# Kernel optimization log

Hardware: AMD Instinct MI355X
Metric: run time of the kernel (lower is better)

The kernel has to match this reference:

```python
import jax, jax.numpy as jnp
import numpy as np

N, F_NODE, F_EDGE = 1024, 64, 32
F_IN = 2 * F_NODE + F_EDGE  # 160


def setup_inputs() -> dict:
    key = jax.random.key(0)
    ks = jax.random.split(key, 6)
    H = jax.random.normal(ks[0], (N, F_NODE), dtype=jnp.float32)
    A = jax.random.randint(ks[1], (N, N), 0, 2).astype(jnp.float32)
    E = jax.random.normal(ks[2], (N, N, F_EDGE), dtype=jnp.float32)
    # params: reset_parameters_uniform -> U(-s, s), s = 1/sqrt(dim0)
    s = 1.0 / np.sqrt(F_IN)
    W = jax.random.uniform(ks[3], (F_IN, F_NODE), jnp.float32, -s, s)
    W_att = jax.random.uniform(ks[4], (F_IN, F_NODE), jnp.float32, -s, s)
    sb = 1.0 / np.sqrt(F_NODE)
    bias = jax.random.uniform(ks[5], (F_NODE,), jnp.float32, -sb, sb)
    return {"H": H, "A": A, "E": E, "W": W, "W_att": W_att, "bias": bias}


def reference(H, A, E, W, W_att, bias):
    n = H.shape[0]
    # all-pairs concat: HE[a,b] = [H[a], H[b], E[a,b]]  -> [N, N, 2F+Fe]
    H_row = jnp.broadcast_to(H[:, None, :], (n, n, H.shape[1]))  # H2: repeat over dim 1
    H_col = jnp.broadcast_to(H[None, :, :], (n, n, H.shape[1]))  # H1: repeat over dim 0
    HE = jnp.concatenate([H_row, H_col, E], axis=2) * A[:, :, None]
    Hp = jnp.einsum('abi,ij->abj', HE, W) + bias
    Ha = jnp.einsum('abi,ij->abj', HE, W_att) + bias
    gated = jax.nn.relu(Hp) * jax.nn.sigmoid(Ha)
    return jnp.sum(gated, axis=1)
```

## Files before the change

kernel.cpp:

```cpp
#include <hip/hip_runtime.h>

#define NN 1024
#define FN 64
#define FE 32
#define FIN 160

#pragma clang diagnostic ignored "-Waddress-space-conversion"

typedef __bf16 bf16x8 __attribute__((ext_vector_type(8)));
typedef short  short8 __attribute__((ext_vector_type(8)));
typedef float  f32x4  __attribute__((ext_vector_type(4)));
typedef __attribute__((address_space(1))) const unsigned int gu32;
typedef __attribute__((address_space(3))) unsigned int lu32;

static __device__ __forceinline__ unsigned short f2b(float x){
    unsigned int u = __float_as_uint(x);
    unsigned int r = (u + 0x7fffu + ((u >> 16) & 1u)) >> 16;
    return (unsigned short)r;
}

static __device__ __forceinline__ float fast_sigmoid(float y){
    return __builtin_amdgcn_rcpf(1.0f + __expf(-y));
}

static __device__ __forceinline__ bf16x8 ldfrag(const unsigned short* p){
    return __builtin_bit_cast(bf16x8, *(const short8*)(p));
}

static __device__ __forceinline__ unsigned packtrunc(float lo, float hi){
    return __builtin_amdgcn_perm(__float_as_uint(hi), __float_as_uint(lo), 0x07060302u);
}

#define MF(A,B,C) __builtin_amdgcn_mfma_f32_16x16x32_bf16((A),(B),(C),0,0,0)

__global__ void prep(const float* __restrict__ H, const float* __restrict__ W,
                     const float* __restrict__ Wa,
                     unsigned short* __restrict__ Hb,
                     unsigned short* __restrict__ WtE,
                     unsigned short* __restrict__ WtA){
    int bid = blockIdx.x, tid = threadIdx.x;
    if (bid < 64){
        int i = (bid*256 + tid)*4;
        float4 v = *(const float4*)(H + i);
        ushort4 o;
        o.x = f2b(v.x); o.y = f2b(v.y); o.z = f2b(v.z); o.w = f2b(v.w);
        *(ushort4*)(Hb + i) = o;
    } else {
        const float* src = (bid == 64) ? W : Wa;
        unsigned short* dst = (bid == 64) ? WtE : WtA;
        for (int idx = tid; idx < FIN*FN; idx += 256){
            int k = idx >> 6, j = idx & 63;
            dst[j*FIN + k] = f2b(src[idx]);
        }
    }
}

#define STAGE(buf_, su_) do {                                               \
    const float* gt_ = E + (size_t)a*(NN*FE) + (su_)*2048;                  \
    _Pragma("unroll")                                                       \
    for (int is_ = 0; is_ < 2; is_++){                                      \
        int L_   = is_*256 + tid;                                           \
        int row_ = ((L_>>8)&1)*32 + ((L_>>7)&1)*16 + (L_ & 15);             \
        int src_ = row_*32 + ((((L_>>4)&3)*2 + ((L_>>6)&1))*4);             \
        __builtin_amdgcn_global_load_lds(                                   \
            (gu32*)(gt_ + src_),                                            \
            (lu32*)(&Et[buf_][is_*1024 + wave*256]), 16, 0, 0);             \
    }                                                                       \
} while(0)

#define COMPMT(buf_, su_, mt_) do {                                         \
    const float* tp_ = &Et[buf_][(mh*2 + (mt_))*512 + quad*64 + col*4];     \
    float4 v0_ = *(const float4*)(tp_);                                     \
    float4 v1_ = *(const float4*)(tp_ + 256);                               \
    int gr_ = (su_)*64 + mh*32 + (mt_)*16 + col;                            \
    bf16x8 hh0_ = ldfrag(Hb + gr_*FN + quad*8);                             \
    bf16x8 hh1_ = ldfrag(Hb + gr_*FN + 32 + quad*8);                        \
    int4 pk_;                                                               \
    pk_.x = (int)packtrunc(v0_.x, v0_.y);                                   \
    pk_.y = (int)packtrunc(v0_.z, v0_.w);                                   \
    pk_.z = (int)packtrunc(v1_.x, v1_.y);                                   \
    pk_.w = (int)packtrunc(v1_.z, v1_.w);                                   \
    bf16x8 ef_ = __builtin_bit_cast(bf16x8, pk_);                           \
    _Pragma("unroll")                                                       \
    for (int tl = 0; tl < 2; tl++){                                         \
        f32x4 pw_ = MF(ef_, Bw[tl][2], MF(hh1_, Bw[tl][1],                  \
                     MF(hh0_, Bw[tl][0], cw[tl])));                         \
        f32x4 pa_ = MF(ef_, Ba[tl][2], MF(hh1_, Ba[tl][1],                  \
                     MF(hh0_, Ba[tl][0], ca[tl])));                         \
        _Pragma("unroll")                                                   \
        for (int r4 = 0; r4 < 4; r4++){                                     \
            float am_ = amask[(su_)*64 + mh*32 + (mt_)*16 + quad*4 + r4];   \
            float f_  = fmaxf(pw_[r4], 0.f) * fast_sigmoid(pa_[r4]);        \
            acc[tl] += am_ * f_;                                            \
        }                                                                   \
    }                                                                       \
} while(0)

__global__ __launch_bounds__(256, 4) void mga_fused(
    const float* __restrict__ A,
    const float* __restrict__ E,
    const unsigned short* __restrict__ Hb,
    const unsigned short* __restrict__ WtE, const unsigned short* __restrict__ WtA,
    const float* __restrict__ bias, float* __restrict__ out)
{
    int a    = blockIdx.x;
    int tid  = threadIdx.x;
    int wave = tid >> 6, lane = tid & 63;
    int col  = lane & 15, quad = lane >> 4;
    int half = wave >> 1, mh = wave & 1;

    __shared__ float Et[4][2048];
    __shared__ float amask[NN];
    __shared__ int wsum[4];
    float* red = (float*)Et;

    int b0 = wave*256 + lane*4;
    float4 av = *(const float4*)(A + (size_t)a*NN + b0);

    bf16x8 Bw[2][3], Ba[2][3];
    #pragma unroll
    for (int tl = 0; tl < 2; tl++){
        int n = (2*half + tl)*16 + col;
        #pragma unroll
        for (int sg = 0; sg < 3; sg++){
            Bw[tl][sg] = ldfrag(WtE + n*FIN + (sg+2)*32 + quad*8);
            Ba[tl][sg] = ldfrag(WtA + n*FIN + (sg+2)*32 + quad*8);
        }
    }

    bf16x8 ha0 = ldfrag(Hb + a*FN + quad*8);
    bf16x8 ha1 = ldfrag(Hb + a*FN + 32 + quad*8);
    f32x4 cw[2], ca[2];
    float acc[2] = {0.f, 0.f};
    #pragma unroll
    for (int tl = 0; tl < 2; tl++){
        int n = (2*half + tl)*16 + col;
        float bj = bias[n];
        f32x4 cb = {bj, bj, bj, bj};
        bf16x8 w0 = ldfrag(WtE + n*FIN + quad*8);
        bf16x8 w1 = ldfrag(WtE + n*FIN + 32 + quad*8);
        cw[tl] = MF(ha1, w1, MF(ha0, w0, cb));
        w0 = ldfrag(WtA + n*FIN + quad*8);
        w1 = ldfrag(WtA + n*FIN + 32 + quad*8);
        ca[tl] = MF(ha1, w1, MF(ha0, w0, cb));
    }

    *(float4*)(amask + b0) = av;
    int m = 0;
    m += (av.x != 0.f) ? 1 : 0;
    m += (av.y != 0.f) ? 1 : 0;
    m += (av.z != 0.f) ? 1 : 0;
    m += (av.w != 0.f) ? 1 : 0;
    #pragma unroll
    for (int d = 1; d < 64; d <<= 1) m += __shfl_xor(m, d, 64);
    if (lane == 0) wsum[wave] = m;

    STAGE(0, 0);
    STAGE(1, 1);
    __syncthreads();
    int c1 = wsum[0] + wsum[1] + wsum[2] + wsum[3];

    #pragma unroll
    for (int su = 0; su < 16; su++){
        int buf = su & 3;
        if (su + 2 < 16) STAGE((su + 2) & 3, su + 2);
        if (su < 14)      { asm volatile("s_waitcnt vmcnt(4)" ::: "memory"); }
        else if (su == 14){ asm volatile("s_waitcnt vmcnt(2)" ::: "memory"); }
        else              { asm volatile("s_waitcnt vmcnt(0)" ::: "memory"); }
        __builtin_amdgcn_s_barrier();
        COMPMT(buf, su, 0);
        COMPMT(buf, su, 1);
    }

    #pragma unroll
    for (int tl = 0; tl < 2; tl++)
        red[(wave*4 + quad)*FN + (2*half + tl)*16 + col] = acc[tl];
    __syncthreads();
    if (tid < FN){
        int rbase = (tid >= 32) ? 8 : 0;
        float sum = 0.f;
        #pragma unroll
        for (int r = 0; r < 8; r++) sum += red[(rbase + r)*FN + tid];
        float bj = bias[tid];
        float g0 = fmaxf(bj, 0.f) * fast_sigmoid(bj);
        out[(size_t)a*FN + tid] = sum + (float)(NN - c1) * g0;
    }
}

extern "C" void kernel_launch(void* const* d_in, const int* in_sizes, int n_in,
                              void* d_out, int out_size, void* d_ws, size_t ws_size,
                              hipStream_t stream) {
    const float* H    = (const float*)d_in[0];
    const float* A    = (const float*)d_in[1];
    const float* E    = (const float*)d_in[2];
    const float* W    = (const float*)d_in[3];
    const float* Wa   = (const float*)d_in[4];
    const float* bias = (const float*)d_in[5];
    float* out = (float*)d_out;

    unsigned short* Hb   = (unsigned short*)d_ws;
    unsigned short* WtE  = Hb + NN*FN;
    unsigned short* WtA  = WtE + FN*FIN;

    prep     <<<dim3(66), dim3(256), 0, stream>>>(H, W, Wa, Hb, WtE, WtA);
    mga_fused<<<dim3(NN), dim3(256), 0, stream>>>(A, E, Hb, WtE, WtA, bias, out);
}
```

Baseline: 233.0 us.

## Precompute per-node H projections and drop H MFMAs from inner loop

```diff
diff --git a/kernel.cpp b/kernel.cpp
--- a/kernel.cpp
+++ b/kernel.cpp
@@ -55,6 +55,45 @@
     }
 }
 
+__global__ void prep2(const unsigned short* __restrict__ Hb,
+                      const unsigned short* __restrict__ WtE,
+                      const unsigned short* __restrict__ WtA,
+                      const float* __restrict__ bias,
+                      float* __restrict__ U1, float* __restrict__ V1,
+                      float* __restrict__ U2t, float* __restrict__ V2t){
+    int tid = threadIdx.x, wave = tid >> 6, lane = tid & 63;
+    int col = lane & 15, quad = lane >> 4;
+    int r0  = blockIdx.x*64 + wave*16;
+    bf16x8 h0 = ldfrag(Hb + (r0 + col)*FN + quad*8);
+    bf16x8 h1 = ldfrag(Hb + (r0 + col)*FN + 32 + quad*8);
+    #pragma unroll
+    for (int jt = 0; jt < 4; jt++){
+        int n = jt*16 + col;
+        float bj = bias[n];
+        f32x4 cb = {bj, bj, bj, bj};
+        f32x4 z  = {0.f, 0.f, 0.f, 0.f};
+        bf16x8 b0 = ldfrag(WtE + n*FIN + quad*8);
+        bf16x8 b1 = ldfrag(WtE + n*FIN + 32 + quad*8);
+        f32x4 u1 = MF(h1, b1, MF(h0, b0, cb));
+        b0 = ldfrag(WtE + n*FIN + 64 + quad*8);
+        b1 = ldfrag(WtE + n*FIN + 96 + quad*8);
+        f32x4 u2 = MF(h1, b1, MF(h0, b0, z));
+        b0 = ldfrag(WtA + n*FIN + quad*8);
+        b1 = ldfrag(WtA + n*FIN + 32 + quad*8);
+        f32x4 v1 = MF(h1, b1, MF(h0, b0, cb));
+        b0 = ldfrag(WtA + n*FIN + 64 + quad*8);
+        b1 = ldfrag(WtA + n*FIN + 96 + quad*8);
+        f32x4 v2 = MF(h1, b1, MF(h0, b0, z));
+        #pragma unroll
+        for (int r = 0; r < 4; r++){
+            U1[(r0 + quad*4 + r)*FN + n] = u1[r];
+            V1[(r0 + quad*4 + r)*FN + n] = v1[r];
+        }
+        *(f32x4*)(U2t + (size_t)n*NN + r0 + quad*4) = u2;
+        *(f32x4*)(V2t + (size_t)n*NN + r0 + quad*4) = v2;
+    }
+}
+
 #define STAGE(buf_, su_) do {                                               \
     const float* gt_ = E + (size_t)a*(NN*FE) + (su_)*2048;                  \
     _Pragma("unroll")                                                       \
@@ -72,9 +111,7 @@
     const float* tp_ = &Et[buf_][(mh*2 + (mt_))*512 + quad*64 + col*4];     \
     float4 v0_ = *(const float4*)(tp_);                                     \
     float4 v1_ = *(const float4*)(tp_ + 256);                               \
-    int gr_ = (su_)*64 + mh*32 + (mt_)*16 + col;                            \
-    bf16x8 hh0_ = ldfrag(Hb + gr_*FN + quad*8);                             \
-    bf16x8 hh1_ = ldfrag(Hb + gr_*FN + 32 + quad*8);                        \
+    int g0_ = (su_)*64 + mh*32 + (mt_)*16 + quad*4;                         \
     int4 pk_;                                                               \
     pk_.x = (int)packtrunc(v0_.x, v0_.y);                                   \
     pk_.y = (int)packtrunc(v0_.z, v0_.w);                                   \
@@ -83,13 +120,20 @@
     bf16x8 ef_ = __builtin_bit_cast(bf16x8, pk_);                           \
     _Pragma("unroll")                                                       \
     for (int tl = 0; tl < 2; tl++){                                         \
-        f32x4 pw_ = MF(ef_, Bw[tl][2], MF(hh1_, Bw[tl][1],                  \
-                     MF(hh0_, Bw[tl][0], cw[tl])));                         \
-        f32x4 pa_ = MF(ef_, Ba[tl][2], MF(hh1_, Ba[tl][1],                  \
-                     MF(hh0_, Ba[tl][0], ca[tl])));                         \
+        int n_ = (2*half + tl)*16 + col;                                    \
+        f32x4 u2_ = *(const f32x4*)(U2t + (size_t)n_*NN + g0_);             \
+        f32x4 w2_ = *(const f32x4*)(V2t + (size_t)n_*NN + g0_);             \
+        f32x4 cw_, ca_;                                                     \
         _Pragma("unroll")                                                   \
         for (int r4 = 0; r4 < 4; r4++){                                     \
-            float am_ = amask[(su_)*64 + mh*32 + (mt_)*16 + quad*4 + r4];   \
+            cw_[r4] = u1s[tl] + u2_[r4];                                    \
+            ca_[r4] = v1s[tl] + w2_[r4];                                    \
+        }                                                                   \
+        f32x4 pw_ = MF(ef_, Bw[tl], cw_);                                   \
+        f32x4 pa_ = MF(ef_, Ba[tl], ca_);                                   \
+        _Pragma("unroll")                                                   \
+        for (int r4 = 0; r4 < 4; r4++){                                     \
+            float am_ = amask[g0_ + r4];                                    \
             float f_  = fmaxf(pw_[r4], 0.f) * fast_sigmoid(pa_[r4]);        \
             acc[tl] += am_ * f_;                                            \
         }                                                                   \
@@ -99,8 +143,9 @@
 __global__ __launch_bounds__(256, 4) void mga_fused(
     const float* __restrict__ A,
     const float* __restrict__ E,
-    const unsigned short* __restrict__ Hb,
     const unsigned short* __restrict__ WtE, const unsigned short* __restrict__ WtA,
+    const float* __restrict__ U1, const float* __restrict__ V1,
+    const float* __restrict__ U2t, const float* __restrict__ V2t,
     const float* __restrict__ bias, float* __restrict__ out)
 {
     int a    = blockIdx.x;
@@ -117,33 +162,15 @@
     int b0 = wave*256 + lane*4;
     float4 av = *(const float4*)(A + (size_t)a*NN + b0);
 
-    bf16x8 Bw[2][3], Ba[2][3];
-    #pragma unroll
-    for (int tl = 0; tl < 2; tl++){
-        int n = (2*half + tl)*16 + col;
-        #pragma unroll
-        for (int sg = 0; sg < 3; sg++){
-            Bw[tl][sg] = ldfrag(WtE + n*FIN + (sg+2)*32 + quad*8);
-            Ba[tl][sg] = ldfrag(WtA + n*FIN + (sg+2)*32 + quad*8);
-        }
-    }
-
-    bf16x8 ha0 = ldfrag(Hb + a*FN + quad*8);
-    bf16x8 ha1 = ldfrag(Hb + a*FN + 32 + quad*8);
-    f32x4 cw[2], ca[2];
+    int n0 = (2*half)*16 + col, n1 = n0 + 16;
+    bf16x8 Bw[2], Ba[2];
+    Bw[0] = ldfrag(WtE + n0*FIN + 128 + quad*8);
+    Bw[1] = ldfrag(WtE + n1*FIN + 128 + quad*8);
+    Ba[0] = ldfrag(WtA + n0*FIN + 128 + quad*8);
+    Ba[1] = ldfrag(WtA + n1*FIN + 128 + quad*8);
+    float u1s[2] = {U1[a*FN + n0], U1[a*FN + n1]};
+    float v1s[2] = {V1[a*FN + n0], V1[a*FN + n1]};
     float acc[2] = {0.f, 0.f};
-    #pragma unroll
-    for (int tl = 0; tl < 2; tl++){
-        int n = (2*half + tl)*16 + col;
-        float bj = bias[n];
-        f32x4 cb = {bj, bj, bj, bj};
-        bf16x8 w0 = ldfrag(WtE + n*FIN + quad*8);
-        bf16x8 w1 = ldfrag(WtE + n*FIN + 32 + quad*8);
-        cw[tl] = MF(ha1, w1, MF(ha0, w0, cb));
-        w0 = ldfrag(WtA + n*FIN + quad*8);
-        w1 = ldfrag(WtA + n*FIN + 32 + quad*8);
-        ca[tl] = MF(ha1, w1, MF(ha0, w0, cb));
-    }
 
     *(float4*)(amask + b0) = av;
     int m = 0;
@@ -201,7 +228,12 @@
     unsigned short* Hb   = (unsigned short*)d_ws;
     unsigned short* WtE  = Hb + NN*FN;
     unsigned short* WtA  = WtE + FN*FIN;
+    float* U1  = (float*)(WtA + FN*FIN);
+    float* V1  = U1 + NN*FN;
+    float* U2t = V1 + NN*FN;
+    float* V2t = U2t + (size_t)FN*NN;
 
     prep     <<<dim3(66), dim3(256), 0, stream>>>(H, W, Wa, Hb, WtE, WtA);
-    mga_fused<<<dim3(NN), dim3(256), 0, stream>>>(A, E, Hb, WtE, WtA, bias, out);
-}
+    prep2    <<<dim3(16), dim3(256), 0, stream>>>(Hb, WtE, WtA, bias, U1, V1, U2t, V2t);
+    mga_fused<<<dim3(NN), dim3(256), 0, stream>>>(A, E, WtE, WtA, U1, V1, U2t, V2t, bias, out);
+}
```

New measurement: 274.0 us. 17.6% more time.
